# Kernel optimization log

Measured on AMD Instinct MI355X. Metric: run time of the kernel, lower is better.

Reference implementation:

```python
import jax, jax.numpy as jnp
import numpy as np
from jax import lax

BETA = 0.5        # Sinkhron beta
N_ITER = 20       # got_iteration
THRESH = 0.1      # P > 0.1 threshold
NL_I = 5          # apply_non_linearity(..., 'elu', i=5)
EPS = 1e-9


def setup_inputs() -> dict:
    key = jax.random.key(0)
    k1, k2 = jax.random.split(key)
    B, N, D = 128, 512, 128
    h = jax.random.normal(k1, (B, N, D), dtype=jnp.float32)
    W0 = jnp.ones((D,), dtype=jnp.float32)
    W1 = jnp.ones((D,), dtype=jnp.float32)
    lengths = jax.random.randint(k2, (B,), 0, N, dtype=jnp.int32)
    return {"h": h, "W0": W0, "W1": W1, "lengths": lengths}


def _forward(h, W0, W1, lengths):
    B, N, D = h.shape
    lengths = jnp.maximum(lengths, 1)
    mask = (jnp.arange(N)[None, :] < lengths[:, None])          # [B, N] bool
    mf = mask.astype(h.dtype)
    mask2 = mf[:, :, None] * mf[:, None, :]                      # [B, N, N]

    # internal_forward: Diag layers with relu between (mlp_act='relu')
    h = h * W0
    h = jax.nn.relu(h)
    h = h * W1

    # cost_matrix_batch_torch: cosine similarity, add identity diag, mask
    hn = h / (jnp.linalg.norm(h, axis=-1, keepdims=True) + 1e-12)
    sim = jnp.einsum('bnd,bmd->bnm', hn, hn)                     # [B, N, N]
    sim = sim + jnp.eye(N, dtype=h.dtype)                        # add_eye_diag
    sim = sim * mask2
    cost = (1.0 - sim) * mask2

    # Sinkhorn with uniform marginals on valid nodes, fixed iterations
    n = lengths.astype(h.dtype)
    mu = mf / n[:, None]                                         # [B, N]
    K = jnp.exp(-cost / BETA) * mask2                            # [B, N, N]

    def body(carry, _):
        u, v = carry
        u = mu / (jnp.einsum('bnm,bm->bn', K, v) + EPS) * mf
        v = mu / (jnp.einsum('bnm,bn->bm', K, u) + EPS) * mf
        return (u, v), None

    (u, v), _ = lax.scan(body, (mf, mf), None, length=N_ITER)
    P = u[:, :, None] * K * v[:, None, :]                        # transport plan

    # P.detach(); scale by number of nodes per graph; threshold
    P = lax.stop_gradient(P)
    P = n[:, None, None] * P
    A = (P > THRESH).astype(h.dtype)
    similarity = A * sim
    # apply_non_linearity 'elu': elu(x*i - i) + 1
    out = jax.nn.elu(similarity * NL_I - NL_I) + 1.0
    return out


def reference(h, W0, W1, lengths):
    return _forward(h, W0, W1, lengths)
```

## Files before the change

### kernel.cpp

```cpp
#include <hip/hip_runtime.h>

#define BB 128
#define NN 512
#define DD 128
#define SLOT_STRIDE 544

__global__ __launch_bounds__(256) void hn_kernel(const float* __restrict__ h,
                                                 const float* __restrict__ W0,
                                                 const float* __restrict__ W1,
                                                 float* __restrict__ hn) {
    int wave = (int)((blockIdx.x * blockDim.x + threadIdx.x) >> 6);
    int lane = threadIdx.x & 63;
    const float2* h2 = (const float2*)(h + (size_t)wave * DD);
    float2 w0 = ((const float2*)W0)[lane];
    float2 w1 = ((const float2*)W1)[lane];
    float2 x = h2[lane];
    float p0 = fmaxf(x.x * w0.x, 0.0f) * w1.x;
    float p1 = fmaxf(x.y * w0.y, 0.0f) * w1.y;
    float ss = p0 * p0 + p1 * p1;
#pragma unroll
    for (int m = 32; m; m >>= 1) ss += __shfl_xor(ss, m);
    float inv = 1.0f / (sqrtf(ss) + 1e-12f);
    float2 o;
    o.x = p0 * inv;
    o.y = p1 * inv;
    ((float2*)(hn + (size_t)wave * DD))[lane] = o;
}

#define KC 32
__global__ __launch_bounds__(256) void sim_kernel(const float* __restrict__ hn,
                                                  const int* __restrict__ lengths,
                                                  float* __restrict__ K) {
    __shared__ float As[KC][132];
    __shared__ float Bs[KC][132];
    __shared__ int pre[BB + 1];
    int tid = threadIdx.x;
    if (tid == 0) {
        int acc = 0;
        for (int b = 0; b < BB; b++) {
            pre[b] = acc;
            int len = max(lengths[b], 1);
            int nt = (len + 127) >> 7;
            acc += nt * nt;
        }
        pre[BB] = acc;
    }
    __syncthreads();
    int total = pre[BB];

    int lr = tid >> 3;
    int lk = (tid & 7) << 2;
    int tx = tid & 15, ty = tid >> 4;

    for (int t = blockIdx.x; t < total; t += gridDim.x) {
        int lo = 0, hi = BB;
        while (lo + 1 < hi) {
            int mid = (lo + hi) >> 1;
            if (pre[mid] <= t) lo = mid; else hi = mid;
        }
        int b = lo;
        int local = t - pre[b];
        int len = max(lengths[b], 1);
        int nt = (len + 127) >> 7;
        int ti = local / nt;
        int tj = local - ti * nt;
        int r0 = ti << 7, c0 = tj << 7;
        const float* base = hn + (size_t)b * NN * DD;
        float acc[8][8] = {};

        for (int kc = 0; kc < DD; kc += KC) {
#pragma unroll
            for (int rr = 0; rr < 128; rr += 32) {
                float4 a = *(const float4*)(base + (size_t)(r0 + lr + rr) * DD + kc + lk);
                As[lk + 0][lr + rr] = a.x; As[lk + 1][lr + rr] = a.y;
                As[lk + 2][lr + rr] = a.z; As[lk + 3][lr + rr] = a.w;
                float4 bb = *(const float4*)(base + (size_t)(c0 + lr + rr) * DD + kc + lk);
                Bs[lk + 0][lr + rr] = bb.x; Bs[lk + 1][lr + rr] = bb.y;
                Bs[lk + 2][lr + rr] = bb.z; Bs[lk + 3][lr + rr] = bb.w;
            }
            __syncthreads();
#pragma unroll
            for (int kk = 0; kk < KC; kk++) {
                float4 a0 = *(const float4*)&As[kk][ty * 8];
                float4 a1 = *(const float4*)&As[kk][ty * 8 + 4];
                float4 b0 = *(const float4*)&Bs[kk][tx * 4];
                float4 b1 = *(const float4*)&Bs[kk][64 + tx * 4];
                float ar[8] = {a0.x, a0.y, a0.z, a0.w, a1.x, a1.y, a1.z, a1.w};
                float bc[8] = {b0.x, b0.y, b0.z, b0.w, b1.x, b1.y, b1.z, b1.w};
#pragma unroll
                for (int r = 0; r < 8; r++)
#pragma unroll
                    for (int c = 0; c < 8; c++)
                        acc[r][c] = fmaf(ar[r], bc[c], acc[r][c]);
            }
            __syncthreads();
        }
        float* out = K + (size_t)b * NN * NN;
#pragma unroll
        for (int r = 0; r < 8; r++) {
            int i = r0 + ty * 8 + r;
            if (i >= len) continue;
#pragma unroll
            for (int cg = 0; cg < 2; cg++) {
                int j0 = c0 + cg * 64 + tx * 4;
                if (j0 >= len) continue;
                float vv[4];
#pragma unroll
                for (int c = 0; c < 4; c++) {
                    float s = acc[r][cg * 4 + c] + ((i == j0 + c) ? 1.0f : 0.0f);
                    vv[c] = expf(2.0f * s - 2.0f);
                }
                float4 o;
                o.x = vv[0]; o.y = vv[1]; o.z = vv[2]; o.w = vv[3];
                *(float4*)(out + (size_t)i * NN + j0) = o;
            }
        }
    }
}

__device__ __forceinline__ float dot8(float4 A, float4 B, float4 x0, float4 x1) {
    float d = fmaf(A.x, x0.x, fmaf(A.y, x0.y, fmaf(A.z, x0.z, A.w * x0.w)));
    return fmaf(B.x, x1.x, fmaf(B.y, x1.y, fmaf(B.z, x1.z, fmaf(B.w, x1.w, d))));
}

#define ROWS22(X) X(0) X(1) X(2) X(3) X(4) X(5) X(6) X(7) X(8) X(9) X(10) \
    X(11) X(12) X(13) X(14) X(15) X(16) X(17) X(18) X(19) X(20) X(21)

__global__ __launch_bounds__(512, 2) void coop_sink(const float* __restrict__ K,
                                                    float* __restrict__ u_buf,
                                                    float* __restrict__ v_buf,
                                                    const int* __restrict__ lengths,
                                                    float* __restrict__ slots) {
    __shared__ float xb[NN];
    __shared__ float pv[8 * NN];
    __shared__ int Sh[BB], Pre[BB];

    int g = blockIdx.x;
    int tid = threadIdx.x;

    if (tid == 0) {
        int need[BB]; int ssum = 0;
        for (int m = 0; m < BB; m++) {
            int L = max(lengths[m], 1);
            need[m] = (L + 175) / 176;
            ssum += need[m];
        }
        while (ssum > 256) {
            int best = 0, bv = need[0];
            for (int m = 1; m < BB; m++)
                if (need[m] > bv) { bv = need[m]; best = m; }
            need[best]--; ssum--;
        }
        int acc = 0;
        for (int m = 0; m < BB; m++) { Pre[m] = acc; Sh[m] = need[m]; acc += need[m]; }
    }
    __syncthreads();

    int m = -1;
    for (int mm = 0; mm < BB; mm++)
        if (g >= Pre[mm] && g < Pre[mm] + Sh[mm]) { m = mm; break; }
    if (m < 0) return;
    int b = m;
    int jbase = Pre[m];
    int q = g - jbase;
    int S = Sh[m];

    int len = max(lengths[b], 1);
    int len4 = (len + 3) & ~3;
    int rpq = (len + S - 1) / S;
    int r_lo = q * rpq;
    int nrows = min(len - r_lo, rpq);
    if (nrows < 0) nrows = 0;
    float inv_n = 1.0f / (float)len;

    int w = tid >> 6, l = tid & 63;
    int c0 = 4 * l, c1 = 256 + 4 * l;
    bool a0 = c0 < len4, a1 = c1 < len4;
    const float* Kb = K + (size_t)b * NN * NN;

    xb[tid] = (tid < len) ? 1.0f : 0.0f;

#define DECL(o) float4 kA##o = {0,0,0,0}, kB##o = {0,0,0,0};
    ROWS22(DECL)
#undef DECL
#define FILL_ROW(o)                                                          \
    {                                                                        \
        int i_ = w + 8 * (o);                                                \
        if (i_ < nrows) {                                                    \
            const float* g0_ = Kb + (size_t)(r_lo + i_) * NN;                \
            if (a0) kA##o = *(const float4*)(g0_ + c0);                      \
            if (a1) kB##o = *(const float4*)(g0_ + c1);                      \
        }                                                                    \
    }
    ROWS22(FILL_ROW)
#undef FILL_ROW

    __syncthreads();

    for (int t = 0; t < 20; t++) {
        float4 xv0 = *(const float4*)(xb + c0);
        float4 xv1 = *(const float4*)(xb + c1);
        float4 pa = {0, 0, 0, 0}, pb = {0, 0, 0, 0};

#define DOT(o) float d##o = dot8(kA##o, kB##o, xv0, xv1);
        ROWS22(DOT)
#undef DOT
#pragma unroll
        for (int mm = 32; mm; mm >>= 1) {
#define BF(o) d##o += __shfl_xor(d##o, mm);
            ROWS22(BF)
#undef BF
        }
#define RC(o) float uu##o = inv_n / (d##o + 1e-9f);
        ROWS22(RC)
#undef RC
#define ACC_ROW(o)                                                           \
    pa.x = fmaf(kA##o.x, uu##o, pa.x); pa.y = fmaf(kA##o.y, uu##o, pa.y);    \
    pa.z = fmaf(kA##o.z, uu##o, pa.z); pa.w = fmaf(kA##o.w, uu##o, pa.w);    \
    pb.x = fmaf(kB##o.x, uu##o, pb.x); pb.y = fmaf(kB##o.y, uu##o, pb.y);    \
    pb.z = fmaf(kB##o.z, uu##o, pb.z); pb.w = fmaf(kB##o.w, uu##o, pb.w);
        ROWS22(ACC_ROW)
#undef ACC_ROW
        if (t == 19 && l == 0) {
            float* ub = u_buf + (size_t)b * NN + r_lo + w;
#define ST(o) if (w + 8 * (o) < nrows) ub[8 * (o)] = uu##o;
            ROWS22(ST)
#undef ST
        }

        for (int i = 176 + w; i < nrows; i += 8) {
            const float* g0 = Kb + (size_t)(r_lo + i) * NN;
            float4 A = {0, 0, 0, 0}, B = {0, 0, 0, 0};
            if (a0) A = *(const float4*)(g0 + c0);
            if (a1) B = *(const float4*)(g0 + c1);
            float d = dot8(A, B, xv0, xv1);
#pragma unroll
            for (int mm = 32; mm; mm >>= 1) d += __shfl_xor(d, mm);
            float uu = inv_n / (d + 1e-9f);
            pa.x = fmaf(A.x, uu, pa.x); pa.y = fmaf(A.y, uu, pa.y);
            pa.z = fmaf(A.z, uu, pa.z); pa.w = fmaf(A.w, uu, pa.w);
            pb.x = fmaf(B.x, uu, pb.x); pb.y = fmaf(B.y, uu, pb.y);
            pb.z = fmaf(B.z, uu, pb.z); pb.w = fmaf(B.w, uu, pb.w);
            if (t == 19 && l == 0) u_buf[(size_t)b * NN + r_lo + i] = uu;
        }

        *(float4*)(pv + w * NN + c0) = pa;
        *(float4*)(pv + w * NN + c1) = pb;
        __syncthreads();
        float* slotp = slots + ((size_t)(t & 1) * 512 + g) * SLOT_STRIDE;
        int c = tid;
        float s0 = pv[c] + pv[NN + c] + pv[2 * NN + c] + pv[3 * NN + c] +
                   pv[4 * NN + c] + pv[5 * NN + c] + pv[6 * NN + c] + pv[7 * NN + c];
        if (S > 1) {
            __hip_atomic_store(slotp + c, s0, __ATOMIC_RELAXED, __HIP_MEMORY_SCOPE_AGENT);
            asm volatile("s_waitcnt vmcnt(0)" ::: "memory");
        }
        __syncthreads();
        if (S > 1 && tid == 0)
            __hip_atomic_store((int*)(slotp + 512), t + 1, __ATOMIC_RELAXED,
                               __HIP_MEMORY_SCOPE_AGENT);
        if (tid < S && tid != q) {
            const int* tagp = (const int*)(slots +
                ((size_t)(t & 1) * 512 + (size_t)(jbase + tid)) * SLOT_STRIDE + 512);
            while (__hip_atomic_load(tagp, __ATOMIC_RELAXED, __HIP_MEMORY_SCOPE_AGENT) != t + 1)
                __builtin_amdgcn_s_sleep(1);
        }
        __syncthreads();

        const float* sbase = slots + ((size_t)(t & 1) * 512) * SLOT_STRIDE;
        float t0 = s0;
        for (int s = 1; s < S; s++) {
            int k = q + s; if (k >= S) k -= S;
            t0 += __hip_atomic_load(sbase + (size_t)(jbase + k) * SLOT_STRIDE + c,
                                    __ATOMIC_RELAXED, __HIP_MEMORY_SCOPE_AGENT);
        }
        float v0 = (c < len) ? (inv_n / (t0 + 1e-9f)) : 0.0f;
        if (t < 19) {
            xb[c] = v0;
        } else if (c >= r_lo && c < r_lo + nrows) {
            v_buf[(size_t)b * NN + c] = v0;
        }
        __syncthreads();
    }
}

__global__ __launch_bounds__(256) void epi_kernel(float* __restrict__ io,
                                                  const float* __restrict__ u,
                                                  const float* __restrict__ v,
                                                  const int* __restrict__ lengths) {
    const float E5 = 0.006737946999085467f;
    size_t idx = (size_t)blockIdx.x * 256 + threadIdx.x;
    int b = (int)(idx >> 16);
    int r = (int)(idx >> 7) & (NN - 1);
    int c4 = ((int)idx & 127) << 2;
    int len = max(lengths[b], 1);
    float4 o;
    if (r >= len || c4 >= len) {
        o.x = E5; o.y = E5; o.z = E5; o.w = E5;
        ((float4*)io)[idx] = o;
        return;
    }
    float4 k = ((float4*)io)[idx];
    float ui = u[(size_t)b * NN + r];
    float4 vv = *(const float4*)(v + (size_t)b * NN + c4);
    float t = (float)len * ui;
    float kv[4] = {k.x, k.y, k.z, k.w};
    float vj[4] = {vv.x, vv.y, vv.z, vv.w};
    float ov[4];
#pragma unroll
    for (int c = 0; c < 4; c++) {
        float Kc = kv[c];
        float P = t * Kc * vj[c];
        bool valid = (c4 + c) < len;
        if (valid && P > 0.1f) {
            float x = 2.5f * logf(Kc);
            ov[c] = (x > 0.0f) ? (x + 1.0f) : expf(x);
        } else {
            ov[c] = E5;
        }
    }
    o.x = ov[0]; o.y = ov[1]; o.z = ov[2]; o.w = ov[3];
    ((float4*)io)[idx] = o;
}

extern "C" void kernel_launch(void* const* d_in, const int* in_sizes, int n_in,
                              void* d_out, int out_size, void* d_ws, size_t ws_size,
                              hipStream_t stream) {
    const float* h = (const float*)d_in[0];
    const float* W0 = (const float*)d_in[1];
    const float* W1 = (const float*)d_in[2];
    const int* lengths = (const int*)d_in[3];
    float* K = (float*)d_out;

    char* ws = (char*)d_ws;
    float* hn = (float*)ws;
    size_t off = (size_t)BB * NN * DD * 4;
    float* u = (float*)(ws + off);     off += (size_t)BB * NN * 4;
    float* v = (float*)(ws + off);     off += (size_t)BB * NN * 4;
    float* slots = (float*)(ws + off); off += (size_t)2 * 512 * SLOT_STRIDE * 4;

    hn_kernel<<<BB * NN / 4, 256, 0, stream>>>(h, W0, W1, hn);
    sim_kernel<<<1024, 256, 0, stream>>>(hn, lengths, K);

    coop_sink<<<256, 512, 0, stream>>>(K, u, v, lengths, slots);

    epi_kernel<<<(unsigned)((size_t)BB * NN * NN / 4 / 256), 256, 0, stream>>>(K, u, v, lengths);
}
```

Measured before the change: 377.8 us.

## Fuse similarity GEMM and exp into Sinkhorn kernel, computing K in registers

Removes the separate sim_kernel and computes each block's K rows directly inside coop_sink. It uses an LDS-staged FP32 GEMM over hn, applies exp, writes K out for the epilogue, and keeps the values in registers for the Sinkhorn loop. This drops one launch and the global read-back of K before iterating. In exchange it adds 32KB of LDS, which may reduce occupancy, and the GEMM now runs only on the 256 Sinkhorn blocks with less tile reuse than the dedicated kernel.

```diff
diff --git a/kernel.cpp b/kernel.cpp
--- a/kernel.cpp
+++ b/kernel.cpp
@@ -27,97 +27,6 @@
     ((float2*)(hn + (size_t)wave * DD))[lane] = o;
 }
 
-#define KC 32
-__global__ __launch_bounds__(256) void sim_kernel(const float* __restrict__ hn,
-                                                  const int* __restrict__ lengths,
-                                                  float* __restrict__ K) {
-    __shared__ float As[KC][132];
-    __shared__ float Bs[KC][132];
-    __shared__ int pre[BB + 1];
-    int tid = threadIdx.x;
-    if (tid == 0) {
-        int acc = 0;
-        for (int b = 0; b < BB; b++) {
-            pre[b] = acc;
-            int len = max(lengths[b], 1);
-            int nt = (len + 127) >> 7;
-            acc += nt * nt;
-        }
-        pre[BB] = acc;
-    }
-    __syncthreads();
-    int total = pre[BB];
-
-    int lr = tid >> 3;
-    int lk = (tid & 7) << 2;
-    int tx = tid & 15, ty = tid >> 4;
-
-    for (int t = blockIdx.x; t < total; t += gridDim.x) {
-        int lo = 0, hi = BB;
-        while (lo + 1 < hi) {
-            int mid = (lo + hi) >> 1;
-            if (pre[mid] <= t) lo = mid; else hi = mid;
-        }
-        int b = lo;
-        int local = t - pre[b];
-        int len = max(lengths[b], 1);
-        int nt = (len + 127) >> 7;
-        int ti = local / nt;
-        int tj = local - ti * nt;
-        int r0 = ti << 7, c0 = tj << 7;
-        const float* base = hn + (size_t)b * NN * DD;
-        float acc[8][8] = {};
-
-        for (int kc = 0; kc < DD; kc += KC) {
-#pragma unroll
-            for (int rr = 0; rr < 128; rr += 32) {
-                float4 a = *(const float4*)(base + (size_t)(r0 + lr + rr) * DD + kc + lk);
-                As[lk + 0][lr + rr] = a.x; As[lk + 1][lr + rr] = a.y;
-                As[lk + 2][lr + rr] = a.z; As[lk + 3][lr + rr] = a.w;
-                float4 bb = *(const float4*)(base + (size_t)(c0 + lr + rr) * DD + kc + lk);
-                Bs[lk + 0][lr + rr] = bb.x; Bs[lk + 1][lr + rr] = bb.y;
-                Bs[lk + 2][lr + rr] = bb.z; Bs[lk + 3][lr + rr] = bb.w;
-            }
-            __syncthreads();
-#pragma unroll
-            for (int kk = 0; kk < KC; kk++) {
-                float4 a0 = *(const float4*)&As[kk][ty * 8];
-                float4 a1 = *(const float4*)&As[kk][ty * 8 + 4];
-                float4 b0 = *(const float4*)&Bs[kk][tx * 4];
-                float4 b1 = *(const float4*)&Bs[kk][64 + tx * 4];
-                float ar[8] = {a0.x, a0.y, a0.z, a0.w, a1.x, a1.y, a1.z, a1.w};
-                float bc[8] = {b0.x, b0.y, b0.z, b0.w, b1.x, b1.y, b1.z, b1.w};
-#pragma unroll
-                for (int r = 0; r < 8; r++)
-#pragma unroll
-                    for (int c = 0; c < 8; c++)
-                        acc[r][c] = fmaf(ar[r], bc[c], acc[r][c]);
-            }
-            __syncthreads();
-        }
-        float* out = K + (size_t)b * NN * NN;
-#pragma unroll
-        for (int r = 0; r < 8; r++) {
-            int i = r0 + ty * 8 + r;
-            if (i >= len) continue;
-#pragma unroll
-            for (int cg = 0; cg < 2; cg++) {
-                int j0 = c0 + cg * 64 + tx * 4;
-                if (j0 >= len) continue;
-                float vv[4];
-#pragma unroll
-                for (int c = 0; c < 4; c++) {
-                    float s = acc[r][cg * 4 + c] + ((i == j0 + c) ? 1.0f : 0.0f);
-                    vv[c] = expf(2.0f * s - 2.0f);
-                }
-                float4 o;
-                o.x = vv[0]; o.y = vv[1]; o.z = vv[2]; o.w = vv[3];
-                *(float4*)(out + (size_t)i * NN + j0) = o;
-            }
-        }
-    }
-}
-
 __device__ __forceinline__ float dot8(float4 A, float4 B, float4 x0, float4 x1) {
     float d = fmaf(A.x, x0.x, fmaf(A.y, x0.y, fmaf(A.z, x0.z, A.w * x0.w)));
     return fmaf(B.x, x1.x, fmaf(B.y, x1.y, fmaf(B.z, x1.z, fmaf(B.w, x1.w, d))));
@@ -126,13 +35,15 @@
 #define ROWS22(X) X(0) X(1) X(2) X(3) X(4) X(5) X(6) X(7) X(8) X(9) X(10) \
     X(11) X(12) X(13) X(14) X(15) X(16) X(17) X(18) X(19) X(20) X(21)
 
-__global__ __launch_bounds__(512, 2) void coop_sink(const float* __restrict__ K,
+__global__ __launch_bounds__(512, 2) void coop_sink(const float* __restrict__ hnG,
+                                                    float* __restrict__ Kio,
                                                     float* __restrict__ u_buf,
                                                     float* __restrict__ v_buf,
                                                     const int* __restrict__ lengths,
                                                     float* __restrict__ slots) {
     __shared__ float xb[NN];
     __shared__ float pv[8 * NN];
+    __shared__ float hnT[16][NN];
     __shared__ int Sh[BB], Pre[BB];
 
     int g = blockIdx.x;
@@ -176,25 +87,127 @@
     int w = tid >> 6, l = tid & 63;
     int c0 = 4 * l, c1 = 256 + 4 * l;
     bool a0 = c0 < len4, a1 = c1 < len4;
-    const float* Kb = K + (size_t)b * NN * NN;
+    const float* hnb = hnG + (size_t)b * NN * DD;
+    float* Kb = Kio + (size_t)b * NN * NN;
 
     xb[tid] = (tid < len) ? 1.0f : 0.0f;
+
+    int omax = (nrows > w) ? ((nrows - w + 7) >> 3) : 0;
+    if (omax > 22) omax = 22;
 
 #define DECL(o) float4 kA##o = {0,0,0,0}, kB##o = {0,0,0,0};
     ROWS22(DECL)
 #undef DECL
-#define FILL_ROW(o)                                                          \
-    {                                                                        \
-        int i_ = w + 8 * (o);                                                \
-        if (i_ < nrows) {                                                    \
-            const float* g0_ = Kb + (size_t)(r_lo + i_) * NN;                \
-            if (a0) kA##o = *(const float4*)(g0_ + c0);                      \
-            if (a1) kB##o = *(const float4*)(g0_ + c1);                      \
-        }                                                                    \
-    }
-    ROWS22(FILL_ROW)
-#undef FILL_ROW
-
+
+    float (*hnRl)[16] = (float (*)[16])pv;
+    for (int kc = 0; kc < DD; kc += 16) {
+        __syncthreads();
+#pragma unroll
+        for (int gg = 0; gg < 4; gg++) {
+            int f = tid + (gg << 9);
+            int col = f >> 2, g4 = (f & 3) << 2;
+            float4 t4 = *(const float4*)(hnb + (size_t)col * DD + kc + g4);
+            hnT[g4 + 0][col] = t4.x; hnT[g4 + 1][col] = t4.y;
+            hnT[g4 + 2][col] = t4.z; hnT[g4 + 3][col] = t4.w;
+        }
+        for (int f = tid; f < 176 * 4; f += 512) {
+            int row = f >> 2, g4 = (f & 3) << 2;
+            int gr = r_lo + row;
+            float4 t4 = {0, 0, 0, 0};
+            if (row < nrows && gr < NN)
+                t4 = *(const float4*)(hnb + (size_t)gr * DD + kc + g4);
+            *(float4*)&hnRl[row][g4] = t4;
+        }
+        __syncthreads();
+        for (int kk = 0; kk < 16; kk++) {
+            float4 B0 = *(const float4*)&hnT[kk][c0];
+#define GEMM_A(o)                                                            \
+            if ((o) < omax) {                                                \
+                float a_ = hnRl[w + 8 * (o)][kk];                            \
+                kA##o.x = fmaf(a_, B0.x, kA##o.x);                           \
+                kA##o.y = fmaf(a_, B0.y, kA##o.y);                           \
+                kA##o.z = fmaf(a_, B0.z, kA##o.z);                           \
+                kA##o.w = fmaf(a_, B0.w, kA##o.w);                           \
+            }
+            ROWS22(GEMM_A)
+#undef GEMM_A
+            if (a1) {
+                float4 B1 = *(const float4*)&hnT[kk][c1];
+#define GEMM_B(o)                                                            \
+                if ((o) < omax) {                                            \
+                    float a_ = hnRl[w + 8 * (o)][kk];                        \
+                    kB##o.x = fmaf(a_, B1.x, kB##o.x);                       \
+                    kB##o.y = fmaf(a_, B1.y, kB##o.y);                       \
+                    kB##o.z = fmaf(a_, B1.z, kB##o.z);                       \
+                    kB##o.w = fmaf(a_, B1.w, kB##o.w);                       \
+                }
+                ROWS22(GEMM_B)
+#undef GEMM_B
+            }
+        }
+    }
+#define FIN_ROW(o)                                                           \
+    if ((o) < omax) {                                                        \
+        int gi_ = r_lo + w + 8 * (o);                                        \
+        kA##o.x = expf(2.0f * (kA##o.x + ((gi_ == c0 + 0) ? 1.0f : 0.0f)) - 2.0f); \
+        kA##o.y = expf(2.0f * (kA##o.y + ((gi_ == c0 + 1) ? 1.0f : 0.0f)) - 2.0f); \
+        kA##o.z = expf(2.0f * (kA##o.z + ((gi_ == c0 + 2) ? 1.0f : 0.0f)) - 2.0f); \
+        kA##o.w = expf(2.0f * (kA##o.w + ((gi_ == c0 + 3) ? 1.0f : 0.0f)) - 2.0f); \
+        kB##o.x = expf(2.0f * (kB##o.x + ((gi_ == c1 + 0) ? 1.0f : 0.0f)) - 2.0f); \
+        kB##o.y = expf(2.0f * (kB##o.y + ((gi_ == c1 + 1) ? 1.0f : 0.0f)) - 2.0f); \
+        kB##o.z = expf(2.0f * (kB##o.z + ((gi_ == c1 + 2) ? 1.0f : 0.0f)) - 2.0f); \
+        kB##o.w = expf(2.0f * (kB##o.w + ((gi_ == c1 + 3) ? 1.0f : 0.0f)) - 2.0f); \
+        if (a0) *(float4*)(Kb + (size_t)gi_ * NN + c0) = kA##o;              \
+        if (a1) *(float4*)(Kb + (size_t)gi_ * NN + c1) = kB##o;              \
+    }
+    ROWS22(FIN_ROW)
+#undef FIN_ROW
+
+    if (nrows > 176) {
+        const float* b0p = hnb + (size_t)(c0 + 0) * DD;
+        const float* b1p = hnb + (size_t)(c0 + 1) * DD;
+        const float* b2p = hnb + (size_t)(c0 + 2) * DD;
+        const float* b3p = hnb + (size_t)(c0 + 3) * DD;
+        const float* b4p = hnb + (size_t)(c1 + 0) * DD;
+        const float* b5p = hnb + (size_t)(c1 + 1) * DD;
+        const float* b6p = hnb + (size_t)(c1 + 2) * DD;
+        const float* b7p = hnb + (size_t)(c1 + 3) * DD;
+        for (int i = 176 + w; i < nrows; i += 8) {
+            int gi = r_lo + i;
+            const float* rowp = hnb + (size_t)gi * DD;
+            float4 accA = {0, 0, 0, 0}, accB = {0, 0, 0, 0};
+            for (int kc = 0; kc < DD; kc += 4) {
+                float4 a4 = *(const float4*)(rowp + kc);
+                float4 p0 = *(const float4*)(b0p + kc);
+                float4 p1 = *(const float4*)(b1p + kc);
+                float4 p2 = *(const float4*)(b2p + kc);
+                float4 p3 = *(const float4*)(b3p + kc);
+                float4 q0 = *(const float4*)(b4p + kc);
+                float4 q1 = *(const float4*)(b5p + kc);
+                float4 q2 = *(const float4*)(b6p + kc);
+                float4 q3 = *(const float4*)(b7p + kc);
+                accA.x = fmaf(a4.w, p0.w, fmaf(a4.z, p0.z, fmaf(a4.y, p0.y, fmaf(a4.x, p0.x, accA.x))));
+                accA.y = fmaf(a4.w, p1.w, fmaf(a4.z, p1.z, fmaf(a4.y, p1.y, fmaf(a4.x, p1.x, accA.y))));
+                accA.z = fmaf(a4.w, p2.w, fmaf(a4.z, p2.z, fmaf(a4.y, p2.y, fmaf(a4.x, p2.x, accA.z))));
+                accA.w = fmaf(a4.w, p3.w, fmaf(a4.z, p3.z, fmaf(a4.y, p3.y, fmaf(a4.x, p3.x, accA.w))));
+                accB.x = fmaf(a4.w, q0.w, fmaf(a4.z, q0.z, fmaf(a4.y, q0.y, fmaf(a4.x, q0.x, accB.x))));
+                accB.y = fmaf(a4.w, q1.w, fmaf(a4.z, q1.z, fmaf(a4.y, q1.y, fmaf(a4.x, q1.x, accB.y))));
+                accB.z = fmaf(a4.w, q2.w, fmaf(a4.z, q2.z, fmaf(a4.y, q2.y, fmaf(a4.x, q2.x, accB.z))));
+                accB.w = fmaf(a4.w, q3.w, fmaf(a4.z, q3.z, fmaf(a4.y, q3.y, fmaf(a4.x, q3.x, accB.w))));
+            }
+            float4 oA, oB;
+            oA.x = expf(2.0f * (accA.x + ((gi == c0 + 0) ? 1.0f : 0.0f)) - 2.0f);
+            oA.y = expf(2.0f * (accA.y + ((gi == c0 + 1) ? 1.0f : 0.0f)) - 2.0f);
+            oA.z = expf(2.0f * (accA.z + ((gi == c0 + 2) ? 1.0f : 0.0f)) - 2.0f);
+            oA.w = expf(2.0f * (accA.w + ((gi == c0 + 3) ? 1.0f : 0.0f)) - 2.0f);
+            oB.x = expf(2.0f * (accB.x + ((gi == c1 + 0) ? 1.0f : 0.0f)) - 2.0f);
+            oB.y = expf(2.0f * (accB.y + ((gi == c1 + 1) ? 1.0f : 0.0f)) - 2.0f);
+            oB.z = expf(2.0f * (accB.z + ((gi == c1 + 2) ? 1.0f : 0.0f)) - 2.0f);
+            oB.w = expf(2.0f * (accB.w + ((gi == c1 + 3) ? 1.0f : 0.0f)) - 2.0f);
+            if (a0) *(float4*)(Kb + (size_t)gi * NN + c0) = oA;
+            if (a1) *(float4*)(Kb + (size_t)gi * NN + c1) = oB;
+        }
+    }
     __syncthreads();
 
     for (int t = 0; t < 20; t++) {
@@ -340,9 +353,8 @@
     float* slots = (float*)(ws + off); off += (size_t)2 * 512 * SLOT_STRIDE * 4;
 
     hn_kernel<<<BB * NN / 4, 256, 0, stream>>>(h, W0, W1, hn);
-    sim_kernel<<<1024, 256, 0, stream>>>(hn, lengths, K);
-
-    coop_sink<<<256, 512, 0, stream>>>(K, u, v, lengths, slots);
+
+    coop_sink<<<256, 512, 0, stream>>>(hn, K, u, v, lengths, slots);
 
     epi_kernel<<<(unsigned)((size_t)BB * NN * NN / 4 / 256), 256, 0, stream>>>(K, u, v, lengths);
 }
```

New measurement: 526.3 us. 1.39x slower.

## Fuse epilogue into Sinkhorn kernel using register-cached K rows

Applied to the files above, without the earlier changes.

The separate epilogue pass that re-read the full K matrix plus u/v buffers is folded into the persistent Sinkhorn kernel. Each block computes the final output for its own rows straight from the K values already held in registers, and uses shared-memory u for the overflow rows. A small pad kernel fills rows beyond each graph's length before Sinkhorn runs. The intent is to avoid one full read of K and the u/v round trip through global memory, at the cost of more register pressure and a serial tail inside the cooperative kernel.

```diff
diff --git a/kernel.cpp b/kernel.cpp
--- a/kernel.cpp
+++ b/kernel.cpp
@@ -118,21 +118,43 @@
     }
 }
 
+__global__ __launch_bounds__(256) void pad_kernel(float* __restrict__ io,
+                                                  const int* __restrict__ lengths) {
+    const float E5 = 0.006737946999085467f;
+    size_t idx = (size_t)blockIdx.x * 256 + threadIdx.x;
+    int b = (int)(idx >> 16);
+    int r = (int)(idx >> 7) & (NN - 1);
+    int len = max(lengths[b], 1);
+    if (r < len) return;
+    float4 o;
+    o.x = E5; o.y = E5; o.z = E5; o.w = E5;
+    ((float4*)io)[idx] = o;
+}
+
 __device__ __forceinline__ float dot8(float4 A, float4 B, float4 x0, float4 x1) {
     float d = fmaf(A.x, x0.x, fmaf(A.y, x0.y, fmaf(A.z, x0.z, A.w * x0.w)));
     return fmaf(B.x, x1.x, fmaf(B.y, x1.y, fmaf(B.z, x1.z, fmaf(B.w, x1.w, d))));
 }
 
+__device__ __forceinline__ float outf(float tt, float Kc, float vj, bool valid) {
+    const float E5 = 0.006737946999085467f;
+    float P = tt * Kc * vj;
+    if (valid && P > 0.1f) {
+        float x = 2.5f * logf(Kc);
+        return (x > 0.0f) ? (x + 1.0f) : expf(x);
+    }
+    return E5;
+}
+
 #define ROWS22(X) X(0) X(1) X(2) X(3) X(4) X(5) X(6) X(7) X(8) X(9) X(10) \
     X(11) X(12) X(13) X(14) X(15) X(16) X(17) X(18) X(19) X(20) X(21)
 
-__global__ __launch_bounds__(512, 2) void coop_sink(const float* __restrict__ K,
-                                                    float* __restrict__ u_buf,
-                                                    float* __restrict__ v_buf,
+__global__ __launch_bounds__(512, 2) void coop_sink(float* __restrict__ K,
                                                     const int* __restrict__ lengths,
                                                     float* __restrict__ slots) {
     __shared__ float xb[NN];
     __shared__ float pv[8 * NN];
+    __shared__ float uS[NN];
     __shared__ int Sh[BB], Pre[BB];
 
     int g = blockIdx.x;
@@ -176,7 +198,7 @@
     int w = tid >> 6, l = tid & 63;
     int c0 = 4 * l, c1 = 256 + 4 * l;
     bool a0 = c0 < len4, a1 = c1 < len4;
-    const float* Kb = K + (size_t)b * NN * NN;
+    float* Kb = K + (size_t)b * NN * NN;
 
     xb[tid] = (tid < len) ? 1.0f : 0.0f;
 
@@ -197,36 +219,27 @@
 
     __syncthreads();
 
-    for (int t = 0; t < 20; t++) {
-        float4 xv0 = *(const float4*)(xb + c0);
-        float4 xv1 = *(const float4*)(xb + c1);
-        float4 pa = {0, 0, 0, 0}, pb = {0, 0, 0, 0};
+#define PHASE_A_CACHED                                                       \
+    ROWS22(DOT)                                                              \
+    _Pragma("unroll")                                                        \
+    for (int mm2 = 32; mm2; mm2 >>= 1) { ROWS22(BF2) }                       \
+    ROWS22(RC) ROWS22(ACC_ROW)
 
 #define DOT(o) float d##o = dot8(kA##o, kB##o, xv0, xv1);
-        ROWS22(DOT)
-#undef DOT
-#pragma unroll
-        for (int mm = 32; mm; mm >>= 1) {
-#define BF(o) d##o += __shfl_xor(d##o, mm);
-            ROWS22(BF)
-#undef BF
-        }
+#define BF2(o) d##o += __shfl_xor(d##o, mm2);
 #define RC(o) float uu##o = inv_n / (d##o + 1e-9f);
-        ROWS22(RC)
-#undef RC
 #define ACC_ROW(o)                                                           \
     pa.x = fmaf(kA##o.x, uu##o, pa.x); pa.y = fmaf(kA##o.y, uu##o, pa.y);    \
     pa.z = fmaf(kA##o.z, uu##o, pa.z); pa.w = fmaf(kA##o.w, uu##o, pa.w);    \
     pb.x = fmaf(kB##o.x, uu##o, pb.x); pb.y = fmaf(kB##o.y, uu##o, pb.y);    \
     pb.z = fmaf(kB##o.z, uu##o, pb.z); pb.w = fmaf(kB##o.w, uu##o, pb.w);
-        ROWS22(ACC_ROW)
-#undef ACC_ROW
-        if (t == 19 && l == 0) {
-            float* ub = u_buf + (size_t)b * NN + r_lo + w;
-#define ST(o) if (w + 8 * (o) < nrows) ub[8 * (o)] = uu##o;
-            ROWS22(ST)
-#undef ST
-        }
+
+    for (int t = 0; t < 19; t++) {
+        float4 xv0 = *(const float4*)(xb + c0);
+        float4 xv1 = *(const float4*)(xb + c1);
+        float4 pa = {0, 0, 0, 0}, pb = {0, 0, 0, 0};
+
+        PHASE_A_CACHED
 
         for (int i = 176 + w; i < nrows; i += 8) {
             const float* g0 = Kb + (size_t)(r_lo + i) * NN;
@@ -235,13 +248,12 @@
             if (a1) B = *(const float4*)(g0 + c1);
             float d = dot8(A, B, xv0, xv1);
 #pragma unroll
-            for (int mm = 32; mm; mm >>= 1) d += __shfl_xor(d, mm);
+            for (int mm2 = 32; mm2; mm2 >>= 1) d += __shfl_xor(d, mm2);
             float uu = inv_n / (d + 1e-9f);
             pa.x = fmaf(A.x, uu, pa.x); pa.y = fmaf(A.y, uu, pa.y);
             pa.z = fmaf(A.z, uu, pa.z); pa.w = fmaf(A.w, uu, pa.w);
             pb.x = fmaf(B.x, uu, pb.x); pb.y = fmaf(B.y, uu, pb.y);
             pb.z = fmaf(B.z, uu, pb.z); pb.w = fmaf(B.w, uu, pb.w);
-            if (t == 19 && l == 0) u_buf[(size_t)b * NN + r_lo + i] = uu;
         }
 
         *(float4*)(pv + w * NN + c0) = pa;
@@ -275,52 +287,113 @@
                                     __ATOMIC_RELAXED, __HIP_MEMORY_SCOPE_AGENT);
         }
         float v0 = (c < len) ? (inv_n / (t0 + 1e-9f)) : 0.0f;
-        if (t < 19) {
-            xb[c] = v0;
-        } else if (c >= r_lo && c < r_lo + nrows) {
-            v_buf[(size_t)b * NN + c] = v0;
-        }
-        __syncthreads();
-    }
-}
-
-__global__ __launch_bounds__(256) void epi_kernel(float* __restrict__ io,
-                                                  const float* __restrict__ u,
-                                                  const float* __restrict__ v,
-                                                  const int* __restrict__ lengths) {
-    const float E5 = 0.006737946999085467f;
-    size_t idx = (size_t)blockIdx.x * 256 + threadIdx.x;
-    int b = (int)(idx >> 16);
-    int r = (int)(idx >> 7) & (NN - 1);
-    int c4 = ((int)idx & 127) << 2;
-    int len = max(lengths[b], 1);
-    float4 o;
-    if (r >= len || c4 >= len) {
-        o.x = E5; o.y = E5; o.z = E5; o.w = E5;
-        ((float4*)io)[idx] = o;
-        return;
-    }
-    float4 k = ((float4*)io)[idx];
-    float ui = u[(size_t)b * NN + r];
-    float4 vv = *(const float4*)(v + (size_t)b * NN + c4);
-    float t = (float)len * ui;
-    float kv[4] = {k.x, k.y, k.z, k.w};
-    float vj[4] = {vv.x, vv.y, vv.z, vv.w};
-    float ov[4];
-#pragma unroll
-    for (int c = 0; c < 4; c++) {
-        float Kc = kv[c];
-        float P = t * Kc * vj[c];
-        bool valid = (c4 + c) < len;
-        if (valid && P > 0.1f) {
-            float x = 2.5f * logf(Kc);
-            ov[c] = (x > 0.0f) ? (x + 1.0f) : expf(x);
-        } else {
-            ov[c] = E5;
-        }
-    }
-    o.x = ov[0]; o.y = ov[1]; o.z = ov[2]; o.w = ov[3];
-    ((float4*)io)[idx] = o;
+        xb[c] = v0;
+        __syncthreads();
+    }
+
+    {
+        float4 xv0 = *(const float4*)(xb + c0);
+        float4 xv1 = *(const float4*)(xb + c1);
+        float4 pa = {0, 0, 0, 0}, pb = {0, 0, 0, 0};
+
+        PHASE_A_CACHED
+
+        for (int i = 176 + w; i < nrows; i += 8) {
+            const float* g0 = Kb + (size_t)(r_lo + i) * NN;
+            float4 A = {0, 0, 0, 0}, B = {0, 0, 0, 0};
+            if (a0) A = *(const float4*)(g0 + c0);
+            if (a1) B = *(const float4*)(g0 + c1);
+            float d = dot8(A, B, xv0, xv1);
+#pragma unroll
+            for (int mm2 = 32; mm2; mm2 >>= 1) d += __shfl_xor(d, mm2);
+            float uu = inv_n / (d + 1e-9f);
+            pa.x = fmaf(A.x, uu, pa.x); pa.y = fmaf(A.y, uu, pa.y);
+            pa.z = fmaf(A.z, uu, pa.z); pa.w = fmaf(A.w, uu, pa.w);
+            pb.x = fmaf(B.x, uu, pb.x); pb.y = fmaf(B.y, uu, pb.y);
+            pb.z = fmaf(B.z, uu, pb.z); pb.w = fmaf(B.w, uu, pb.w);
+            uS[i] = uu;
+        }
+
+        *(float4*)(pv + w * NN + c0) = pa;
+        *(float4*)(pv + w * NN + c1) = pb;
+        __syncthreads();
+        float* slotp = slots + ((size_t)1 * 512 + g) * SLOT_STRIDE;
+        int c = tid;
+        float s0 = pv[c] + pv[NN + c] + pv[2 * NN + c] + pv[3 * NN + c] +
+                   pv[4 * NN + c] + pv[5 * NN + c] + pv[6 * NN + c] + pv[7 * NN + c];
+        if (S > 1) {
+            __hip_atomic_store(slotp + c, s0, __ATOMIC_RELAXED, __HIP_MEMORY_SCOPE_AGENT);
+            asm volatile("s_waitcnt vmcnt(0)" ::: "memory");
+        }
+        __syncthreads();
+        if (S > 1 && tid == 0)
+            __hip_atomic_store((int*)(slotp + 512), 20, __ATOMIC_RELAXED,
+                               __HIP_MEMORY_SCOPE_AGENT);
+        if (tid < S && tid != q) {
+            const int* tagp = (const int*)(slots +
+                ((size_t)1 * 512 + (size_t)(jbase + tid)) * SLOT_STRIDE + 512);
+            while (__hip_atomic_load(tagp, __ATOMIC_RELAXED, __HIP_MEMORY_SCOPE_AGENT) != 20)
+                __builtin_amdgcn_s_sleep(1);
+        }
+        __syncthreads();
+
+        const float* sbase = slots + ((size_t)1 * 512) * SLOT_STRIDE;
+        float t0 = s0;
+        for (int s = 1; s < S; s++) {
+            int k = q + s; if (k >= S) k -= S;
+            t0 += __hip_atomic_load(sbase + (size_t)(jbase + k) * SLOT_STRIDE + c,
+                                    __ATOMIC_RELAXED, __HIP_MEMORY_SCOPE_AGENT);
+        }
+        float v0 = (c < len) ? (inv_n / (t0 + 1e-9f)) : 0.0f;
+        xb[c] = v0;
+        __syncthreads();
+
+        float4 w0v = *(const float4*)(xb + c0);
+        float4 w1v = *(const float4*)(xb + c1);
+#define EPI_ROW(o)                                                           \
+        if (w + 8 * (o) < nrows) {                                           \
+            int gi_ = r_lo + w + 8 * (o);                                    \
+            float tt_ = (float)len * uu##o;                                  \
+            float4 oA_, oB_;                                                 \
+            oA_.x = outf(tt_, kA##o.x, w0v.x, c0 + 0 < len);                 \
+            oA_.y = outf(tt_, kA##o.y, w0v.y, c0 + 1 < len);                 \
+            oA_.z = outf(tt_, kA##o.z, w0v.z, c0 + 2 < len);                 \
+            oA_.w = outf(tt_, kA##o.w, w0v.w, c0 + 3 < len);                 \
+            oB_.x = outf(tt_, kB##o.x, w1v.x, c1 + 0 < len);                 \
+            oB_.y = outf(tt_, kB##o.y, w1v.y, c1 + 1 < len);                 \
+            oB_.z = outf(tt_, kB##o.z, w1v.z, c1 + 2 < len);                 \
+            oB_.w = outf(tt_, kB##o.w, w1v.w, c1 + 3 < len);                 \
+            *(float4*)(Kb + (size_t)gi_ * NN + c0) = oA_;                    \
+            *(float4*)(Kb + (size_t)gi_ * NN + c1) = oB_;                    \
+        }
+        ROWS22(EPI_ROW)
+#undef EPI_ROW
+
+        for (int i = 176 + w; i < nrows; i += 8) {
+            int gi = r_lo + i;
+            float tt = (float)len * uS[i];
+            const float* g0 = Kb + (size_t)gi * NN;
+            float4 A = {0, 0, 0, 0}, B = {0, 0, 0, 0};
+            if (a0) A = *(const float4*)(g0 + c0);
+            if (a1) B = *(const float4*)(g0 + c1);
+            float4 oA, oB;
+            oA.x = outf(tt, A.x, w0v.x, c0 + 0 < len);
+            oA.y = outf(tt, A.y, w0v.y, c0 + 1 < len);
+            oA.z = outf(tt, A.z, w0v.z, c0 + 2 < len);
+            oA.w = outf(tt, A.w, w0v.w, c0 + 3 < len);
+            oB.x = outf(tt, B.x, w1v.x, c1 + 0 < len);
+            oB.y = outf(tt, B.y, w1v.y, c1 + 1 < len);
+            oB.z = outf(tt, B.z, w1v.z, c1 + 2 < len);
+            oB.w = outf(tt, B.w, w1v.w, c1 + 3 < len);
+            *(float4*)(Kb + (size_t)gi * NN + c0) = oA;
+            *(float4*)(Kb + (size_t)gi * NN + c1) = oB;
+        }
+    }
+#undef DOT
+#undef BF2
+#undef RC
+#undef ACC_ROW
+#undef PHASE_A_CACHED
 }
 
 extern "C" void kernel_launch(void* const* d_in, const int* in_sizes, int n_in,
@@ -335,14 +408,11 @@
     char* ws = (char*)d_ws;
     float* hn = (float*)ws;
     size_t off = (size_t)BB * NN * DD * 4;
-    float* u = (float*)(ws + off);     off += (size_t)BB * NN * 4;
-    float* v = (float*)(ws + off);     off += (size_t)BB * NN * 4;
     float* slots = (float*)(ws + off); off += (size_t)2 * 512 * SLOT_STRIDE * 4;
 
     hn_kernel<<<BB * NN / 4, 256, 0, stream>>>(h, W0, W1, hn);
     sim_kernel<<<1024, 256, 0, stream>>>(hn, lengths, K);
-
-    coop_sink<<<256, 512, 0, stream>>>(K, u, v, lengths, slots);
-
-    epi_kernel<<<(unsigned)((size_t)BB * NN * NN / 4 / 256), 256, 0, stream>>>(K, u, v, lengths);
-}
+    pad_kernel<<<(unsigned)((size_t)BB * NN * NN / 4 / 256), 256, 0, stream>>>(K, lengths);
+
+    coop_sink<<<256, 512, 0, stream>>>(K, lengths, slots);
+}
```

After: 391.3 us. 3.6% more time.

## Pack iteration tag with partial sums to replace flag-based inter-block barrier

Applied to the files above, without the earlier changes.

Each block now writes its per-column partial sum together with the iteration number as one 64-bit atomic value, instead of writing floats, draining stores, and publishing a separate tag. Consumers spin per element on the tag of the value they read. This drops two __syncthreads, the vmcnt drain and the single-thread flag spin from each of the 20 iterations, so cross-block reduction latency should shrink. The cost is twice the slot memory traffic and per-element polling. Correctness relies on each 64-bit store being atomic.

```diff
diff --git a/kernel.cpp b/kernel.cpp
--- a/kernel.cpp
+++ b/kernel.cpp
@@ -3,7 +3,6 @@
 #define BB 128
 #define NN 512
 #define DD 128
-#define SLOT_STRIDE 544
 
 __global__ __launch_bounds__(256) void hn_kernel(const float* __restrict__ h,
                                                  const float* __restrict__ W0,
@@ -130,7 +129,7 @@
                                                     float* __restrict__ u_buf,
                                                     float* __restrict__ v_buf,
                                                     const int* __restrict__ lengths,
-                                                    float* __restrict__ slots) {
+                                                    unsigned long long* __restrict__ slots64) {
     __shared__ float xb[NN];
     __shared__ float pv[8 * NN];
     __shared__ int Sh[BB], Pre[BB];
@@ -206,8 +205,8 @@
         ROWS22(DOT)
 #undef DOT
 #pragma unroll
-        for (int mm = 32; mm; mm >>= 1) {
-#define BF(o) d##o += __shfl_xor(d##o, mm);
+        for (int mm2 = 32; mm2; mm2 >>= 1) {
+#define BF(o) d##o += __shfl_xor(d##o, mm2);
             ROWS22(BF)
 #undef BF
         }
@@ -235,7 +234,7 @@
             if (a1) B = *(const float4*)(g0 + c1);
             float d = dot8(A, B, xv0, xv1);
 #pragma unroll
-            for (int mm = 32; mm; mm >>= 1) d += __shfl_xor(d, mm);
+            for (int mm2 = 32; mm2; mm2 >>= 1) d += __shfl_xor(d, mm2);
             float uu = inv_n / (d + 1e-9f);
             pa.x = fmaf(A.x, uu, pa.x); pa.y = fmaf(A.y, uu, pa.y);
             pa.z = fmaf(A.z, uu, pa.z); pa.w = fmaf(A.w, uu, pa.w);
@@ -247,32 +246,29 @@
         *(float4*)(pv + w * NN + c0) = pa;
         *(float4*)(pv + w * NN + c1) = pb;
         __syncthreads();
-        float* slotp = slots + ((size_t)(t & 1) * 512 + g) * SLOT_STRIDE;
         int c = tid;
         float s0 = pv[c] + pv[NN + c] + pv[2 * NN + c] + pv[3 * NN + c] +
                    pv[4 * NN + c] + pv[5 * NN + c] + pv[6 * NN + c] + pv[7 * NN + c];
+        unsigned long long* pbase =
+            slots64 + ((size_t)(t & 1) * 512) * 512;
         if (S > 1) {
-            __hip_atomic_store(slotp + c, s0, __ATOMIC_RELAXED, __HIP_MEMORY_SCOPE_AGENT);
-            asm volatile("s_waitcnt vmcnt(0)" ::: "memory");
-        }
-        __syncthreads();
-        if (S > 1 && tid == 0)
-            __hip_atomic_store((int*)(slotp + 512), t + 1, __ATOMIC_RELAXED,
-                               __HIP_MEMORY_SCOPE_AGENT);
-        if (tid < S && tid != q) {
-            const int* tagp = (const int*)(slots +
-                ((size_t)(t & 1) * 512 + (size_t)(jbase + tid)) * SLOT_STRIDE + 512);
-            while (__hip_atomic_load(tagp, __ATOMIC_RELAXED, __HIP_MEMORY_SCOPE_AGENT) != t + 1)
-                __builtin_amdgcn_s_sleep(1);
-        }
-        __syncthreads();
-
-        const float* sbase = slots + ((size_t)(t & 1) * 512) * SLOT_STRIDE;
+            unsigned long long pk =
+                ((unsigned long long)(unsigned)(t + 1) << 32) | __float_as_uint(s0);
+            __hip_atomic_store(pbase + (size_t)g * 512 + c, pk,
+                               __ATOMIC_RELAXED, __HIP_MEMORY_SCOPE_AGENT);
+        }
+
         float t0 = s0;
         for (int s = 1; s < S; s++) {
             int k = q + s; if (k >= S) k -= S;
-            t0 += __hip_atomic_load(sbase + (size_t)(jbase + k) * SLOT_STRIDE + c,
-                                    __ATOMIC_RELAXED, __HIP_MEMORY_SCOPE_AGENT);
+            const unsigned long long* p64 = pbase + (size_t)(jbase + k) * 512 + c;
+            unsigned long long vpk =
+                __hip_atomic_load(p64, __ATOMIC_RELAXED, __HIP_MEMORY_SCOPE_AGENT);
+            while ((unsigned)(vpk >> 32) != (unsigned)(t + 1)) {
+                __builtin_amdgcn_s_sleep(1);
+                vpk = __hip_atomic_load(p64, __ATOMIC_RELAXED, __HIP_MEMORY_SCOPE_AGENT);
+            }
+            t0 += __uint_as_float((unsigned)vpk);
         }
         float v0 = (c < len) ? (inv_n / (t0 + 1e-9f)) : 0.0f;
         if (t < 19) {
@@ -335,14 +331,15 @@
     char* ws = (char*)d_ws;
     float* hn = (float*)ws;
     size_t off = (size_t)BB * NN * DD * 4;
-    float* u = (float*)(ws + off);     off += (size_t)BB * NN * 4;
-    float* v = (float*)(ws + off);     off += (size_t)BB * NN * 4;
-    float* slots = (float*)(ws + off); off += (size_t)2 * 512 * SLOT_STRIDE * 4;
+    float* u = (float*)(ws + off); off += (size_t)BB * NN * 4;
+    float* v = (float*)(ws + off); off += (size_t)BB * NN * 4;
+    unsigned long long* slots64 = (unsigned long long*)(ws + off);
+    off += (size_t)2 * 512 * 512 * 8;
 
     hn_kernel<<<BB * NN / 4, 256, 0, stream>>>(h, W0, W1, hn);
     sim_kernel<<<1024, 256, 0, stream>>>(hn, lengths, K);
 
-    coop_sink<<<256, 512, 0, stream>>>(K, u, v, lengths, slots);
+    coop_sink<<<256, 512, 0, stream>>>(K, u, v, lengths, slots64);
 
     epi_kernel<<<(unsigned)((size_t)BB * NN * NN / 4 / 256), 256, 0, stream>>>(K, u, v, lengths);
 }
```

After: 362.6 us. 4.0% less time.
